# Optimization experiments

Measured on AMD Instinct MI355X. Metric: run time of the kernel, lower is better.

Reference implementation:

```python
import jax, jax.numpy as jnp
import numpy as np

NUM_HEADS = 16
D_K = 8  # == n_qubits


def setup_inputs() -> dict:
    key = jax.random.key(0)
    k1, k2, k3 = jax.random.split(key, 3)
    x = jax.random.normal(k1, (4, 2048, 128), dtype=jnp.float32)
    # trainable RX angles, one per qubit (tq.RX has_params=True)
    theta = jax.random.normal(k2, (D_K,), dtype=jnp.float32)
    # out_proj: Linear(embed_dim, embed_dim, bias=False)
    w_out = jax.random.normal(k3, (128, 128), dtype=jnp.float32) * (1.0 / np.sqrt(128.0))
    return {"x": x, "theta": theta, "w_out": w_out}


def quantum_features(x, theta):
    # x: [b, s, e]. Per head of size d_k: encode RX(x_i), trainable RX(theta_i)
    # (composes to RX(x_i + theta_i)), CNOT ladder [i, i+1], measure PauliZ.
    # Heisenberg picture: Z_w -> Z_0...Z_w, so <Z_w> = prod_{i<=w} cos(x_i + theta_i).
    b, s, e = x.shape
    heads = x.reshape(b, s, NUM_HEADS, D_K)
    return jnp.cumprod(jnp.cos(heads + theta), axis=-1)  # [b, s, h, d_k]


def reference(x, theta, w_out):
    b, s, e = x.shape
    # q == k == v: same shared q_layer applied to the same x three times.
    qkv = quantum_features(x, theta)            # [b, s, h, d_k]
    q = qkv.transpose(0, 2, 1, 3)               # [b, h, s, d_k]
    scores = jnp.einsum('bhqd,bhkd->bhqk', q, q) / np.sqrt(D_K)
    attn = jax.nn.softmax(scores, axis=-1)      # dropout is identity at eval
    out = jnp.einsum('bhqk,bhkd->bhqd', attn, q)
    out = out.transpose(0, 2, 1, 3).reshape(b, s, e)
    return out @ w_out.T
```

## Files before the change

### kernel.cpp

```cpp
#include <hip/hip_runtime.h>

#define BATCH 4
#define SEQ   2048
#define EMB   128
#define NH    16
#define DK    8

#define QSCALE 0.510069726f

typedef _Float16 v4h __attribute__((ext_vector_type(4)));
typedef _Float16 v8h __attribute__((ext_vector_type(8)));
typedef float    v4f __attribute__((ext_vector_type(4)));

#define CHUNK 1024
#define VTP   1032

__global__ void feat_kernel(const float* __restrict__ x,
                            const float* __restrict__ theta,
                            const float* __restrict__ W,
                            _Float16* __restrict__ Fh,
                            _Float16* __restrict__ Qh,
                            _Float16* __restrict__ Wh) {
  __shared__ float Xs[32][132];

  const int tid = threadIdx.x;
  const int b   = blockIdx.x >> 6;
  const int s0  = (blockIdx.x & 63) * 32;

#pragma unroll
  for (int it = 0; it < 4; ++it) {
    const int idx = it * 256 + tid;
    const int r  = idx >> 5;
    const int e4 = idx & 31;
    const float4 v = *(const float4*)(x + ((size_t)b * SEQ + s0 + r) * EMB + e4 * 4);
    *(float4*)&Xs[r][e4 * 4] = v;
  }

  if (tid < 16) {
    const int i4 = blockIdx.x * 64 + tid * 4;
    const float4 w = *(const float4*)(W + i4);
    v4h wh = {(_Float16)w.x, (_Float16)w.y, (_Float16)w.z, (_Float16)w.w};
    *(v4h*)(Wh + i4) = wh;
  }

  float th[DK];
#pragma unroll
  for (int i = 0; i < DK; ++i) th[i] = theta[i];
  __syncthreads();

#pragma unroll
  for (int it = 0; it < 2; ++it) {
    const int id = it * 256 + tid;
    const int s = id & 31;
    const int h = id >> 5;
    const float* xr = &Xs[s][h * 8];
    const float f0 = __cosf(xr[0] + th[0]);
    const float f1 = f0 * __cosf(xr[1] + th[1]);
    const float f2 = f1 * __cosf(xr[2] + th[2]);
    const float f3 = f2 * __cosf(xr[3] + th[3]);
    const float f4 = f3 * __cosf(xr[4] + th[4]);
    const float f5 = f4 * __cosf(xr[5] + th[5]);
    const float f6 = f5 * __cosf(xr[6] + th[6]);
    const float f7 = f6 * __cosf(xr[7] + th[7]);
    const size_t off = (((size_t)(b * NH + h)) * SEQ + s0 + s) * DK;
    v8h fv = {(_Float16)f0, (_Float16)f1, (_Float16)f2, (_Float16)f3,
              (_Float16)f4, (_Float16)f5, (_Float16)f6, (_Float16)f7};
    v8h qv = {(_Float16)(f0 * QSCALE), (_Float16)(f1 * QSCALE),
              (_Float16)(f2 * QSCALE), (_Float16)(f3 * QSCALE),
              (_Float16)(f4 * QSCALE), (_Float16)(f5 * QSCALE),
              (_Float16)(f6 * QSCALE), (_Float16)(f7 * QSCALE)};
    *(v8h*)(Fh + off) = fv;
    *(v8h*)(Qh + off) = qv;
  }
}

__launch_bounds__(256, 2)
__global__ void attn_kernel(const _Float16* __restrict__ Fh,
                            const _Float16* __restrict__ Qh,
                            _Float16* __restrict__ Ah ) {
  __shared__ __align__(16) _Float16 Kl[CHUNK * 8];
  __shared__ __align__(16) _Float16 VT[16][VTP];

  const int tid  = threadIdx.x;
  const int L    = tid & 63;
  const int wv   = tid >> 6;
  const int quad = L >> 4;
  const int ln   = L & 15;
  const int bh   = blockIdx.x >> 3;
  const int qb   = (blockIdx.x & 7) * 256 + wv * 64;

  const _Float16* __restrict__ fbase = Fh + (size_t)bh * SEQ * DK;
  const _Float16* __restrict__ qbase = Qh + (size_t)bh * SEQ * DK;

  for (int i = tid; i < 8 * VTP / 4; i += 256) {
    v4h v = (i < VTP / 4) ? (v4h){(_Float16)1.f, (_Float16)1.f,
                                  (_Float16)1.f, (_Float16)1.f}
                          : (v4h){0, 0, 0, 0};
    *(v4h*)(&VT[8][0] + i * 4) = v;
  }

  v4h qf[4];
#pragma unroll
  for (int t = 0; t < 4; ++t) {
    v4h q = {0, 0, 0, 0};
    const int qrow = qb + t * 16 + ln;
    if (quad < 2) q = *(const v4h*)(qbase + (size_t)qrow * DK + quad * 4);
    qf[t] = q;
  }

  v4f acc[4];
#pragma unroll
  for (int t = 0; t < 4; ++t) acc[t] = (v4f){0.f, 0.f, 0.f, 0.f};
  const v4f zf = (v4f){0.f, 0.f, 0.f, 0.f};

  for (int c = 0; c < 2; ++c) {
    if (c) __syncthreads();
    const _Float16* fc = fbase + (size_t)c * CHUNK * DK;
#pragma unroll
    for (int it = 0; it < 4; ++it) {
      const int key = it * 256 + tid;
      *(float4*)&Kl[key * 8] = *(const float4*)(fc + key * 8);
    }
    {
      const int k4 = tid * 4;
      const v8h r0 = *(const v8h*)(fc + (size_t)(k4 + 0) * 8);
      const v8h r1 = *(const v8h*)(fc + (size_t)(k4 + 1) * 8);
      const v8h r2 = *(const v8h*)(fc + (size_t)(k4 + 2) * 8);
      const v8h r3 = *(const v8h*)(fc + (size_t)(k4 + 3) * 8);
#pragma unroll
      for (int d = 0; d < 8; ++d) {
        v4h w = {r0[d], r1[d], r2[d], r3[d]};
        *(v4h*)&VT[d][k4] = w;
      }
    }
    __syncthreads();

    for (int t16 = 0; t16 < CHUNK / 16; ++t16) {
      const v4h kv = *(const v4h*)&Kl[(t16 * 16 + ln) * 8 + (quad & 1) * 4];
      const v4h kf = (quad < 2) ? kv : (v4h){0, 0, 0, 0};
      const v4h vt = *(const v4h*)&VT[ln][t16 * 16 + quad * 4];
#pragma unroll
      for (int t = 0; t < 4; ++t) {
        const v4f s = __builtin_amdgcn_mfma_f32_16x16x16f16(kf, qf[t], zf, 0, 0, 0);
        v4h pb;
        pb[0] = (_Float16)__builtin_amdgcn_exp2f(s[0]);
        pb[1] = (_Float16)__builtin_amdgcn_exp2f(s[1]);
        pb[2] = (_Float16)__builtin_amdgcn_exp2f(s[2]);
        pb[3] = (_Float16)__builtin_amdgcn_exp2f(s[3]);
        acc[t] = __builtin_amdgcn_mfma_f32_16x16x16f16(vt, pb, acc[t], 0, 0, 0);
      }
    }
  }

  const int b = bh >> 4;
  const int h = bh & 15;
#pragma unroll
  for (int t = 0; t < 4; ++t) {
    const float den = __shfl(acc[t][0], 32 + ln, 64);
    const float inv = 1.0f / den;
    if (quad < 2) {
      const int qrow = qb + t * 16 + ln;
      v4h o = {(_Float16)(acc[t][0] * inv), (_Float16)(acc[t][1] * inv),
               (_Float16)(acc[t][2] * inv), (_Float16)(acc[t][3] * inv)};
      *(v4h*)(Ah + ((size_t)b * SEQ + qrow) * EMB + h * DK + quad * 4) = o;
    }
  }
}

__launch_bounds__(256, 1)
__global__ void proj_kernel(const _Float16* __restrict__ Ah,
                            const _Float16* __restrict__ Wh,
                            float* __restrict__ out) {
  __shared__ __align__(16) _Float16 Ahs[64][136];
  __shared__ __align__(16) _Float16 Whs[128][136];

  const int tid  = threadIdx.x;
  const int L    = tid & 63;
  const int wv   = tid >> 6;
  const int quad = L >> 4;
  const int ln   = L & 15;
  const int rowbase = blockIdx.x * 64;

#pragma unroll
  for (int it = 0; it < 4; ++it) {
    const int idx = it * 256 + tid;
    const int r  = idx >> 4;
    const int c8 = idx & 15;
    *(uint4*)&Ahs[r][c8 * 8] =
        *(const uint4*)(Ah + (size_t)(rowbase + r) * EMB + c8 * 8);
  }
#pragma unroll
  for (int it = 0; it < 8; ++it) {
    const int idx = it * 256 + tid;
    const int n  = idx >> 4;
    const int c8 = idx & 15;
    *(uint4*)&Whs[n][c8 * 8] = *(const uint4*)(Wh + (size_t)n * EMB + c8 * 8);
  }
  __syncthreads();

  v4f acc[8];
#pragma unroll
  for (int nt = 0; nt < 8; ++nt) acc[nt] = (v4f){0.f, 0.f, 0.f, 0.f};

#pragma unroll
  for (int k8 = 0; k8 < 8; ++k8) {
    const v4h af = *(const v4h*)&Ahs[wv * 16 + ln][k8 * 16 + quad * 4];
#pragma unroll
    for (int nt = 0; nt < 8; ++nt) {
      const v4h bf = *(const v4h*)&Whs[nt * 16 + ln][k8 * 16 + quad * 4];
      acc[nt] = __builtin_amdgcn_mfma_f32_16x16x16f16(af, bf, acc[nt], 0, 0, 0);
    }
  }

#pragma unroll
  for (int nt = 0; nt < 8; ++nt) {
    const int col = nt * 16 + ln;
#pragma unroll
    for (int r = 0; r < 4; ++r) {
      out[(size_t)(rowbase + wv * 16 + quad * 4 + r) * EMB + col] = acc[nt][r];
    }
  }
}

extern "C" void kernel_launch(void* const* d_in, const int* in_sizes, int n_in,
                              void* d_out, int out_size, void* d_ws, size_t ws_size,
                              hipStream_t stream) {
  const float* x     = (const float*)d_in[0];
  const float* theta = (const float*)d_in[1];
  const float* w_out = (const float*)d_in[2];
  float* out = (float*)d_out;

  const size_t FSZ = (size_t)BATCH * NH * SEQ * DK;
  _Float16* Fh = (_Float16*)d_ws;
  _Float16* Qh = Fh + FSZ;
  _Float16* Ah = Qh + FSZ;
  _Float16* Wh = Ah + (size_t)BATCH * SEQ * EMB;

  feat_kernel<<<dim3(256), dim3(256), 0, stream>>>(x, theta, w_out, Fh, Qh, Wh);
  attn_kernel<<<dim3(512), dim3(256), 0, stream>>>(Fh, Qh, Ah);
  proj_kernel<<<dim3((BATCH * SEQ) / 64), dim3(256), 0, stream>>>(Ah, Wh, out);
}
```

Measured before the change: 102.9 us.

## Fuse quantum feature computation into attention kernel and convert W in projection

Removes the separate feature kernel. Each attention block now recomputes the cos-cumprod features for its key chunk straight from x, writes them to LDS, and takes its scaled queries from the LDS chunk it already holds. Blocks grow to 512 threads with two query tiles per wave, and W is converted to fp16 inside the projection kernel. This saves a launch and the fp16 feature round trip through global memory, but each (b,h) feature set is recomputed by 8 blocks and x is read with strided 32-byte accesses.

```diff
diff --git a/kernel.cpp b/kernel.cpp
--- a/kernel.cpp
+++ b/kernel.cpp
@@ -8,75 +8,16 @@
 
 #define QSCALE 0.510069726f
 
+typedef _Float16 v2h __attribute__((ext_vector_type(2)));
 typedef _Float16 v4h __attribute__((ext_vector_type(4)));
-typedef _Float16 v8h __attribute__((ext_vector_type(8)));
 typedef float    v4f __attribute__((ext_vector_type(4)));
 
 #define CHUNK 1024
 #define VTP   1032
 
-__global__ void feat_kernel(const float* __restrict__ x,
+__launch_bounds__(512, 4)
+__global__ void attn_kernel(const float* __restrict__ x,
                             const float* __restrict__ theta,
-                            const float* __restrict__ W,
-                            _Float16* __restrict__ Fh,
-                            _Float16* __restrict__ Qh,
-                            _Float16* __restrict__ Wh) {
-  __shared__ float Xs[32][132];
-
-  const int tid = threadIdx.x;
-  const int b   = blockIdx.x >> 6;
-  const int s0  = (blockIdx.x & 63) * 32;
-
-#pragma unroll
-  for (int it = 0; it < 4; ++it) {
-    const int idx = it * 256 + tid;
-    const int r  = idx >> 5;
-    const int e4 = idx & 31;
-    const float4 v = *(const float4*)(x + ((size_t)b * SEQ + s0 + r) * EMB + e4 * 4);
-    *(float4*)&Xs[r][e4 * 4] = v;
-  }
-
-  if (tid < 16) {
-    const int i4 = blockIdx.x * 64 + tid * 4;
-    const float4 w = *(const float4*)(W + i4);
-    v4h wh = {(_Float16)w.x, (_Float16)w.y, (_Float16)w.z, (_Float16)w.w};
-    *(v4h*)(Wh + i4) = wh;
-  }
-
-  float th[DK];
-#pragma unroll
-  for (int i = 0; i < DK; ++i) th[i] = theta[i];
-  __syncthreads();
-
-#pragma unroll
-  for (int it = 0; it < 2; ++it) {
-    const int id = it * 256 + tid;
-    const int s = id & 31;
-    const int h = id >> 5;
-    const float* xr = &Xs[s][h * 8];
-    const float f0 = __cosf(xr[0] + th[0]);
-    const float f1 = f0 * __cosf(xr[1] + th[1]);
-    const float f2 = f1 * __cosf(xr[2] + th[2]);
-    const float f3 = f2 * __cosf(xr[3] + th[3]);
-    const float f4 = f3 * __cosf(xr[4] + th[4]);
-    const float f5 = f4 * __cosf(xr[5] + th[5]);
-    const float f6 = f5 * __cosf(xr[6] + th[6]);
-    const float f7 = f6 * __cosf(xr[7] + th[7]);
-    const size_t off = (((size_t)(b * NH + h)) * SEQ + s0 + s) * DK;
-    v8h fv = {(_Float16)f0, (_Float16)f1, (_Float16)f2, (_Float16)f3,
-              (_Float16)f4, (_Float16)f5, (_Float16)f6, (_Float16)f7};
-    v8h qv = {(_Float16)(f0 * QSCALE), (_Float16)(f1 * QSCALE),
-              (_Float16)(f2 * QSCALE), (_Float16)(f3 * QSCALE),
-              (_Float16)(f4 * QSCALE), (_Float16)(f5 * QSCALE),
-              (_Float16)(f6 * QSCALE), (_Float16)(f7 * QSCALE)};
-    *(v8h*)(Fh + off) = fv;
-    *(v8h*)(Qh + off) = qv;
-  }
-}
-
-__launch_bounds__(256, 2)
-__global__ void attn_kernel(const _Float16* __restrict__ Fh,
-                            const _Float16* __restrict__ Qh,
                             _Float16* __restrict__ Ah ) {
   __shared__ __align__(16) _Float16 Kl[CHUNK * 8];
   __shared__ __align__(16) _Float16 VT[16][VTP];
@@ -86,61 +27,98 @@
   const int wv   = tid >> 6;
   const int quad = L >> 4;
   const int ln   = L & 15;
-  const int bh   = blockIdx.x >> 3;
-  const int qb   = (blockIdx.x & 7) * 256 + wv * 64;
-
-  const _Float16* __restrict__ fbase = Fh + (size_t)bh * SEQ * DK;
-  const _Float16* __restrict__ qbase = Qh + (size_t)bh * SEQ * DK;
-
-  for (int i = tid; i < 8 * VTP / 4; i += 256) {
+  const int bh     = blockIdx.x >> 3;
+  const int qchunk = blockIdx.x & 7;
+  const int qb     = qchunk * 256 + wv * 32;
+  const int b = bh >> 4;
+  const int h = bh & 15;
+
+  float th[DK];
+#pragma unroll
+  for (int i = 0; i < DK; ++i) th[i] = theta[i];
+
+  for (int i = tid; i < 8 * VTP / 4; i += 512) {
     v4h v = (i < VTP / 4) ? (v4h){(_Float16)1.f, (_Float16)1.f,
                                   (_Float16)1.f, (_Float16)1.f}
                           : (v4h){0, 0, 0, 0};
     *(v4h*)(&VT[8][0] + i * 4) = v;
   }
 
-  v4h qf[4];
-#pragma unroll
-  for (int t = 0; t < 4; ++t) {
-    v4h q = {0, 0, 0, 0};
-    const int qrow = qb + t * 16 + ln;
-    if (quad < 2) q = *(const v4h*)(qbase + (size_t)qrow * DK + quad * 4);
-    qf[t] = q;
-  }
-
-  v4f acc[4];
-#pragma unroll
-  for (int t = 0; t < 4; ++t) acc[t] = (v4f){0.f, 0.f, 0.f, 0.f};
+  const int c0 = qchunk >> 2;
+  v4h qf[2];
+  v4f acc[2];
+  acc[0] = (v4f){0.f, 0.f, 0.f, 0.f};
+  acc[1] = (v4f){0.f, 0.f, 0.f, 0.f};
   const v4f zf = (v4f){0.f, 0.f, 0.f, 0.f};
 
-  for (int c = 0; c < 2; ++c) {
-    if (c) __syncthreads();
-    const _Float16* fc = fbase + (size_t)c * CHUNK * DK;
-#pragma unroll
-    for (int it = 0; it < 4; ++it) {
-      const int key = it * 256 + tid;
-      *(float4*)&Kl[key * 8] = *(const float4*)(fc + key * 8);
-    }
+  for (int cc = 0; cc < 2; ++cc) {
+    const int c = cc ? (1 - c0) : c0;
+    if (cc) __syncthreads();
+
     {
-      const int k4 = tid * 4;
-      const v8h r0 = *(const v8h*)(fc + (size_t)(k4 + 0) * 8);
-      const v8h r1 = *(const v8h*)(fc + (size_t)(k4 + 1) * 8);
-      const v8h r2 = *(const v8h*)(fc + (size_t)(k4 + 2) * 8);
-      const v8h r3 = *(const v8h*)(fc + (size_t)(k4 + 3) * 8);
+      const int k2 = tid * 2;
+      const float* xp = x + ((size_t)b * SEQ + c * CHUNK + k2) * EMB + h * DK;
+      const float4 a0 = *(const float4*)(xp);
+      const float4 a1 = *(const float4*)(xp + 4);
+      const float4 b0 = *(const float4*)(xp + EMB);
+      const float4 b1 = *(const float4*)(xp + EMB + 4);
+
+      float r0[8], r1[8];
+      r0[0] = __cosf(a0.x + th[0]);
+      r0[1] = r0[0] * __cosf(a0.y + th[1]);
+      r0[2] = r0[1] * __cosf(a0.z + th[2]);
+      r0[3] = r0[2] * __cosf(a0.w + th[3]);
+      r0[4] = r0[3] * __cosf(a1.x + th[4]);
+      r0[5] = r0[4] * __cosf(a1.y + th[5]);
+      r0[6] = r0[5] * __cosf(a1.z + th[6]);
+      r0[7] = r0[6] * __cosf(a1.w + th[7]);
+      r1[0] = __cosf(b0.x + th[0]);
+      r1[1] = r1[0] * __cosf(b0.y + th[1]);
+      r1[2] = r1[1] * __cosf(b0.z + th[2]);
+      r1[3] = r1[2] * __cosf(b0.w + th[3]);
+      r1[4] = r1[3] * __cosf(b1.x + th[4]);
+      r1[5] = r1[4] * __cosf(b1.y + th[5]);
+      r1[6] = r1[5] * __cosf(b1.z + th[6]);
+      r1[7] = r1[6] * __cosf(b1.w + th[7]);
+
+      _Float16 h0[8], h1[8];
+#pragma unroll
+      for (int i = 0; i < 8; ++i) { h0[i] = (_Float16)r0[i]; h1[i] = (_Float16)r1[i]; }
+
+      union { v4h v[2]; float4 f; } u0, u1;
+      u0.v[0] = (v4h){h0[0], h0[1], h0[2], h0[3]};
+      u0.v[1] = (v4h){h0[4], h0[5], h0[6], h0[7]};
+      u1.v[0] = (v4h){h1[0], h1[1], h1[2], h1[3]};
+      u1.v[1] = (v4h){h1[4], h1[5], h1[6], h1[7]};
+      *(float4*)&Kl[k2 * 8]     = u0.f;
+      *(float4*)&Kl[k2 * 8 + 8] = u1.f;
+
 #pragma unroll
       for (int d = 0; d < 8; ++d) {
-        v4h w = {r0[d], r1[d], r2[d], r3[d]};
-        *(v4h*)&VT[d][k4] = w;
+        v2h w = {h0[d], h1[d]};
+        *(v2h*)&VT[d][k2] = w;
       }
     }
     __syncthreads();
+
+    if (cc == 0) {
+      const v4h qsc = {(_Float16)QSCALE, (_Float16)QSCALE,
+                       (_Float16)QSCALE, (_Float16)QSCALE};
+#pragma unroll
+      for (int t = 0; t < 2; ++t) {
+        const int lrow = qb - c0 * CHUNK + t * 16 + ln;
+        v4h q = {0, 0, 0, 0};
+        if (quad < 2) q = *(const v4h*)&Kl[lrow * 8 + quad * 4];
+        qf[t] = q * qsc;
+      }
+    }
 
     for (int t16 = 0; t16 < CHUNK / 16; ++t16) {
       const v4h kv = *(const v4h*)&Kl[(t16 * 16 + ln) * 8 + (quad & 1) * 4];
       const v4h kf = (quad < 2) ? kv : (v4h){0, 0, 0, 0};
       const v4h vt = *(const v4h*)&VT[ln][t16 * 16 + quad * 4];
 #pragma unroll
-      for (int t = 0; t < 4; ++t) {
+      for (int t = 0; t < 2; ++t) {
         const v4f s = __builtin_amdgcn_mfma_f32_16x16x16f16(kf, qf[t], zf, 0, 0, 0);
         v4h pb;
         pb[0] = (_Float16)__builtin_amdgcn_exp2f(s[0]);
@@ -152,10 +130,8 @@
     }
   }
 
-  const int b = bh >> 4;
-  const int h = bh & 15;
-#pragma unroll
-  for (int t = 0; t < 4; ++t) {
+#pragma unroll
+  for (int t = 0; t < 2; ++t) {
     const float den = __shfl(acc[t][0], 32 + ln, 64);
     const float inv = 1.0f / den;
     if (quad < 2) {
@@ -169,7 +145,7 @@
 
 __launch_bounds__(256, 1)
 __global__ void proj_kernel(const _Float16* __restrict__ Ah,
-                            const _Float16* __restrict__ Wh,
+                            const float* __restrict__ W,
                             float* __restrict__ out) {
   __shared__ __align__(16) _Float16 Ahs[64][136];
   __shared__ __align__(16) _Float16 Whs[128][136];
@@ -190,11 +166,13 @@
         *(const uint4*)(Ah + (size_t)(rowbase + r) * EMB + c8 * 8);
   }
 #pragma unroll
-  for (int it = 0; it < 8; ++it) {
+  for (int it = 0; it < 16; ++it) {
     const int idx = it * 256 + tid;
-    const int n  = idx >> 4;
-    const int c8 = idx & 15;
-    *(uint4*)&Whs[n][c8 * 8] = *(const uint4*)(Wh + (size_t)n * EMB + c8 * 8);
+    const int n  = idx >> 5;
+    const int c4 = idx & 31;
+    const float4 w = *(const float4*)(W + (size_t)n * EMB + c4 * 4);
+    v4h wh = {(_Float16)w.x, (_Float16)w.y, (_Float16)w.z, (_Float16)w.w};
+    *(v4h*)&Whs[n][c4 * 4] = wh;
   }
   __syncthreads();
 
@@ -230,13 +208,9 @@
   const float* w_out = (const float*)d_in[2];
   float* out = (float*)d_out;
 
-  const size_t FSZ = (size_t)BATCH * NH * SEQ * DK;
-  _Float16* Fh = (_Float16*)d_ws;
-  _Float16* Qh = Fh + FSZ;
-  _Float16* Ah = Qh + FSZ;
-  _Float16* Wh = Ah + (size_t)BATCH * SEQ * EMB;
-
-  feat_kernel<<<dim3(256), dim3(256), 0, stream>>>(x, theta, w_out, Fh, Qh, Wh);
-  attn_kernel<<<dim3(512), dim3(256), 0, stream>>>(Fh, Qh, Ah);
-  proj_kernel<<<dim3((BATCH * SEQ) / 64), dim3(256), 0, stream>>>(Ah, Wh, out);
+  _Float16* Ah = (_Float16*)d_ws;
+
+  attn_kernel<<<dim3(512), dim3(512), 0, stream>>>(x, theta, Ah);
+
+  proj_kernel<<<dim3((BATCH * SEQ) / 64), dim3(256), 0, stream>>>(Ah, w_out, out);
 }
```

Measured after the change: 97.89 us. 4.9% less time.
